# Performance work log

Measured on AMD Instinct MI355X. Metric: run time of the kernel, lower is better.

The kernel has to match this reference:

```python
import jax, jax.numpy as jnp
import numpy as np

N, B, I = 64, 32, 1
EMBED, ACT, DETER, STOCH, HIDDEN = 1536, 16, 2048, 512, 1024
EPS = 1e-5


def _ln(x, g, b):
    m = jnp.mean(x, -1, keepdims=True)
    v = jnp.mean((x - m) ** 2, -1, keepdims=True)
    return (x - m) / jnp.sqrt(v + EPS) * g + b


def setup_inputs() -> dict:
    key = jax.random.key(0)
    ks = jax.random.split(key, 24)
    s = 0.02
    d = {
        "embed": jax.random.normal(ks[0], (N, B, EMBED), jnp.float32),
        "action": jax.random.normal(ks[1], (N, B, ACT), jnp.float32),
        "reset": jnp.zeros((N, B), jnp.bool_),
        "h0": jnp.zeros((B * I, DETER), jnp.float32),
        "z0": jnp.zeros((B * I, STOCH), jnp.float32),
        "noises": jax.random.normal(ks[2], (N, B, I, STOCH), jnp.float32),
        # params
        "W_z": jax.random.normal(ks[3], (HIDDEN, STOCH)) * s,
        "b_z": jnp.zeros((HIDDEN,)),
        "W_a": jax.random.normal(ks[4], (HIDDEN, ACT)) * s,
        "ln_in_g": jnp.ones((HIDDEN,)), "ln_in_b": jnp.zeros((HIDDEN,)),
        "gru_Wih": jax.random.normal(ks[5], (3 * DETER, HIDDEN)) * s,
        "gru_Whh": jax.random.normal(ks[6], (3 * DETER, DETER)) * s,
        "gru_bih": jnp.zeros((3 * DETER,)), "gru_bhh": jnp.zeros((3 * DETER,)),
        "W_ph": jax.random.normal(ks[7], (HIDDEN, DETER)) * s,
        "b_ph": jnp.zeros((HIDDEN,)),
        "W_pe": jax.random.normal(ks[8], (HIDDEN, EMBED)) * s,
        "ln_post_g": jnp.ones((HIDDEN,)), "ln_post_b": jnp.zeros((HIDDEN,)),
        "W_post": jax.random.normal(ks[9], (2 * STOCH, HIDDEN)) * s,
        "b_post": jnp.zeros((2 * STOCH,)),
        "W_prh": jax.random.normal(ks[10], (HIDDEN, DETER)) * s,
        "b_prh": jnp.zeros((HIDDEN,)),
        "ln_pr_g": jnp.ones((HIDDEN,)), "ln_pr_b": jnp.zeros((HIDDEN,)),
        "W_pr": jax.random.normal(ks[11], (2 * STOCH, HIDDEN)) * s,
        "b_pr": jnp.zeros((2 * STOCH,)),
    }
    return d


def _core(embed, action, reset, h0, z0, noises,
          W_z, b_z, W_a, ln_in_g, ln_in_b,
          gru_Wih, gru_Whh, gru_bih, gru_bhh,
          W_ph, b_ph, W_pe, ln_post_g, ln_post_b, W_post, b_post,
          W_prh, b_prh, ln_pr_g, ln_pr_b, W_pr, b_pr):
    n, b = embed.shape[:2]
    # expand to (n, b*I, .) ; I == 1
    embeds = embed.reshape(n, b * I, -1)
    actions = action.reshape(n, b * I, -1)
    masks = (~reset).astype(jnp.float32).reshape(n, b * I, 1)
    noise = noises.reshape(n, b * I, -1)

    def step(carry, xs):
        h, z = carry
        e_t, a_t, m_t, n_t = xs
        h = h * m_t
        z = z * m_t
        x = z @ W_z.T + b_z + a_t @ W_a.T
        za = jax.nn.elu(_ln(x, ln_in_g, ln_in_b))
        # torch GRUCell
        gi = za @ gru_Wih.T + gru_bih
        gh = h @ gru_Whh.T + gru_bhh
        gi_r, gi_u, gi_n = jnp.split(gi, 3, -1)
        gh_r, gh_u, gh_n = jnp.split(gh, 3, -1)
        r = jax.nn.sigmoid(gi_r + gh_r)
        u = jax.nn.sigmoid(gi_u + gh_u)
        cand = jnp.tanh(gi_n + r * gh_n)
        h_new = (1.0 - u) * cand + u * h
        x = h_new @ W_ph.T + b_ph + e_t @ W_pe.T
        post_in = jax.nn.elu(_ln(x, ln_post_g, ln_post_b))
        post = post_in @ W_post.T + b_post
        mean, std_raw = jnp.split(post, 2, -1)
        std = jax.nn.softplus(std_raw) + 0.1
        sample = mean + std * n_t
        return (h_new, sample), (post, h_new, sample)

    (h_last, z_last), (posts, states_h, samples) = jax.lax.scan(
        step, (h0, z0), (embeds, actions, masks, noise))

    # batch prior over all h
    x = states_h @ W_prh.T + b_prh
    x = jax.nn.elu(_ln(x, ln_pr_g, ln_pr_b))
    priors = x @ W_pr.T + b_pr
    features = jnp.concatenate([states_h, samples], -1)

    rs = lambda t: t.reshape(n, b, I, -1)
    return rs(priors), rs(posts), rs(samples), rs(features), h_last, z_last


def reference(embed, action, reset, h0, z0, noises,
              W_z, b_z, W_a, ln_in_g, ln_in_b,
              gru_Wih, gru_Whh, gru_bih, gru_bhh,
              W_ph, b_ph, W_pe, ln_post_g, ln_post_b, W_post, b_post,
              W_prh, b_prh, ln_pr_g, ln_pr_b, W_pr, b_pr):
    return _core(embed, action, reset, h0, z0, noises,
                 W_z, b_z, W_a, ln_in_g, ln_in_b,
                 gru_Wih, gru_Whh, gru_bih, gru_bhh,
                 W_ph, b_ph, W_pe, ln_post_g, ln_post_b, W_post, b_post,
                 W_prh, b_prh, ln_pr_g, ln_pr_b, W_pr, b_pr)
```

## Files before the change

kernel.cpp:

```cpp
#include <hip/hip_runtime.h>
#include <hip/hip_bf16.h>
#include <stdint.h>

#define NSTEP 64
#define BATCH 32
#define EMBED_D 1536
#define ACT_D 16
#define DETER 2048
#define STOCH 512
#define HIDDEN 1024
#define FEAT 2560
#define NBLK 256

typedef __attribute__((ext_vector_type(8))) short bf16x8;
typedef __attribute__((ext_vector_type(4))) float f32x4;

#define MFMA16 __builtin_amdgcn_mfma_f32_16x16x32_bf16
#define AGENT __HIP_MEMORY_SCOPE_AGENT

__device__ __forceinline__ float eluf(float x) { return x > 0.f ? x : expf(x) - 1.f; }
__device__ __forceinline__ float sigf(float x) { return 1.f / (1.f + expf(-x)); }
__device__ __forceinline__ unsigned short f2bf(float f) {
    __hip_bfloat16 h = __float2bfloat16(f);
    return __builtin_bit_cast(unsigned short, h);
}
__device__ __forceinline__ float bf2f(unsigned short u) {
    unsigned v = ((unsigned)u) << 16;
    return __builtin_bit_cast(float, v);
}

__device__ __forceinline__ void stc_u32(unsigned* p, unsigned v) {
    __hip_atomic_store(p, v, __ATOMIC_RELAXED, AGENT);
}
__device__ __forceinline__ void stc_u64(unsigned long long* p, unsigned long long v) {
    __hip_atomic_store(p, v, __ATOMIC_RELAXED, AGENT);
}
__device__ __forceinline__ unsigned long long ldc_u64(const unsigned long long* p) {
    return __hip_atomic_load(p, __ATOMIC_RELAXED, AGENT);
}
__device__ __forceinline__ float ldc_f32(const float* p) {
    return __hip_atomic_load(p, __ATOMIC_RELAXED, AGENT);
}
__device__ __forceinline__ int ldc_i32(const int* p) {
    return __hip_atomic_load(p, __ATOMIC_RELAXED, AGENT);
}
__device__ __forceinline__ void stc_i32(int* p, int v) {
    __hip_atomic_store(p, v, __ATOMIC_RELAXED, AGENT);
}
__device__ __forceinline__ bf16x8 ldc_bf8(const unsigned short* p) {
    union { unsigned long long q[2]; bf16x8 v; } u;
    u.q[0] = ldc_u64((const unsigned long long*)p);
    u.q[1] = ldc_u64((const unsigned long long*)(p + 4));
    return u.v;
}
__device__ __forceinline__ ushort4 ldc_us4(const unsigned short* p) {
    unsigned long long q = ldc_u64((const unsigned long long*)p);
    return __builtin_bit_cast(ushort4, q);
}

__device__ __forceinline__ void gbar3(int* flags, int* release, int epoch) {
    asm volatile("s_waitcnt vmcnt(0)" ::: "memory");
    __syncthreads();
    if (blockIdx.x == 0) {
        int tid = threadIdx.x;
        if (tid >= 1 && tid < NBLK) {
            while (ldc_i32(&flags[tid * 32]) < epoch) __builtin_amdgcn_s_sleep(4);
        }
        asm volatile("" ::: "memory");
        __syncthreads();
        if (tid < 32) stc_i32(&release[tid * 32], epoch);
    } else {
        if (threadIdx.x == 0) {
            stc_i32(&flags[blockIdx.x * 32], epoch);
            int* rel = &release[(blockIdx.x & 31) * 32];
            while (ldc_i32(rel) < epoch) __builtin_amdgcn_s_sleep(4);
        }
        asm volatile("" ::: "memory");
        __syncthreads();
    }
}

__global__ __launch_bounds__(256) void k_cvt_all(
    const float* __restrict__ s0, unsigned short* __restrict__ d0,
    const float* __restrict__ s1, unsigned short* __restrict__ d1,
    const float* __restrict__ s2, unsigned short* __restrict__ d2,
    const float* __restrict__ s3, unsigned short* __restrict__ d3,
    const float* __restrict__ s4, unsigned short* __restrict__ d4)
{
    long long e = ((long long)blockIdx.x * 256 + threadIdx.x) * 4;
    const float* src; unsigned short* dst; long long off;
    if (e < 524288)        { src = s0; dst = d0; off = e; }
    else if (e < 6815744)  { src = s1; dst = d1; off = e - 524288; }
    else if (e < 19398656) { src = s2; dst = d2; off = e - 6815744; }
    else if (e < 21495808) { src = s3; dst = d3; off = e - 19398656; }
    else if (e < 22544384) { src = s4; dst = d4; off = e - 21495808; }
    else return;
    float4 v = *reinterpret_cast<const float4*>(src + off);
    ushort4 o;
    o.x = f2bf(v.x); o.y = f2bf(v.y); o.z = f2bf(v.z); o.w = f2bf(v.w);
    *reinterpret_cast<ushort4*>(dst + off) = o;
}

__global__ __launch_bounds__(256) void k_setup(
    const float* __restrict__ h0, const float* __restrict__ z0,
    const uint8_t* __restrict__ reset0,
    float* __restrict__ h0m, unsigned short* __restrict__ h16m0,
    unsigned short* __restrict__ z16m, int* __restrict__ flags)
{
    int gid = blockIdx.x * 256 + threadIdx.x;
    int idx = gid * 4;
    if (idx < BATCH * DETER) {
        int b = idx >> 11;
        float m = reset0[b] ? 0.f : 1.f;
        float4 v = *reinterpret_cast<const float4*>(h0 + idx);
        v.x *= m; v.y *= m; v.z *= m; v.w *= m;
        *reinterpret_cast<float4*>(h0m + idx) = v;
        ushort4 o;
        o.x = f2bf(v.x); o.y = f2bf(v.y); o.z = f2bf(v.z); o.w = f2bf(v.w);
        *reinterpret_cast<ushort4*>(h16m0 + idx) = o;
    } else if (idx < BATCH * DETER + BATCH * STOCH) {
        int zi = idx - BATCH * DETER;
        int b = zi >> 9;
        float m = reset0[b] ? 0.f : 1.f;
        float4 v = *reinterpret_cast<const float4*>(z0 + zi);
        ushort4 o;
        o.x = f2bf(v.x * m); o.y = f2bf(v.y * m); o.z = f2bf(v.z * m); o.w = f2bf(v.w * m);
        *reinterpret_cast<ushort4*>(z16m + zi) = o;
    }
    if (gid < 9216) flags[gid] = 0;
}

__global__ __launch_bounds__(256) void k_preA(
    const float* __restrict__ action, const float* __restrict__ Wa,
    const float* __restrict__ bz, float* __restrict__ preA)
{
    __shared__ float al[16];
    int r = blockIdx.x, t = threadIdx.x;
    if (t < 16) al[t] = action[r * 16 + t];
    __syncthreads();
#pragma unroll
    for (int c = 0; c < 4; ++c) {
        int j = t + c * 256;
        const float* wr = Wa + j * 16;
        float s = bz[j];
#pragma unroll
        for (int k = 0; k < 16; ++k) s += al[k] * wr[k];
        preA[(size_t)r * 1024 + j] = s;
    }
}

__global__ __launch_bounds__(256) void gemm_mfma(
    const float* __restrict__ A, int lda,
    const float* __restrict__ B, int ldb,
    const float* __restrict__ bias,
    float* __restrict__ C, int ldc, int K)
{
    __shared__ unsigned short Alds[64 * 72];
    __shared__ unsigned short Blds[64 * 72];
    int t = threadIdx.x;
    int nb = blockIdx.x, mb = blockIdx.y;
    int w = t >> 6, l = t & 63, l15 = l & 15, kg = l >> 4;
    f32x4 acc[4] = {{0,0,0,0},{0,0,0,0},{0,0,0,0},{0,0,0,0}};
    int srow = t >> 2, skq = (t & 3) * 16;
    const float* Asrc = A + (size_t)(mb * 64 + srow) * lda + skq;
    const float* Bsrc = B + (size_t)(nb * 64 + srow) * ldb + skq;
    unsigned short* Adst = &Alds[srow * 72 + skq];
    unsigned short* Bdst = &Blds[srow * 72 + skq];
    for (int kt = 0; kt < K; kt += 64) {
        __syncthreads();
#pragma unroll
        for (int c = 0; c < 16; c += 4) {
            float4 va = *reinterpret_cast<const float4*>(Asrc + kt + c);
            float4 vb = *reinterpret_cast<const float4*>(Bsrc + kt + c);
            ushort4 oa, ob;
            oa.x = f2bf(va.x); oa.y = f2bf(va.y); oa.z = f2bf(va.z); oa.w = f2bf(va.w);
            ob.x = f2bf(vb.x); ob.y = f2bf(vb.y); ob.z = f2bf(vb.z); ob.w = f2bf(vb.w);
            *reinterpret_cast<ushort4*>(Adst + c) = oa;
            *reinterpret_cast<ushort4*>(Bdst + c) = ob;
        }
        __syncthreads();
#pragma unroll
        for (int ks = 0; ks < 2; ks++) {
            bf16x8 a = *reinterpret_cast<const bf16x8*>(&Alds[(w * 16 + l15) * 72 + ks * 32 + kg * 8]);
#pragma unroll
            for (int nt = 0; nt < 4; nt++) {
                bf16x8 b = *reinterpret_cast<const bf16x8*>(&Blds[(nt * 16 + l15) * 72 + ks * 32 + kg * 8]);
                acc[nt] = MFMA16(a, b, acc[nt], 0, 0, 0);
            }
        }
    }
#pragma unroll
    for (int nt = 0; nt < 4; nt++) {
        int n = nb * 64 + nt * 16 + l15;
        float bv = bias[n];
#pragma unroll
        for (int i = 0; i < 4; i++) {
            C[(size_t)(mb * 64 + w * 16 + kg * 4 + i) * ldc + n] = acc[nt][i] + bv;
        }
    }
}

__global__ __launch_bounds__(256) void ln_elu_rows(
    float* __restrict__ X, const float* __restrict__ g, const float* __restrict__ bb)
{
    __shared__ float sbuf[256], qbuf[256];
    int r = blockIdx.x, t = threadIdx.x;
    float* row = X + (size_t)r * HIDDEN;
    float4 v = reinterpret_cast<const float4*>(row)[t];
    sbuf[t] = (v.x + v.y) + (v.z + v.w);
    qbuf[t] = (v.x * v.x + v.y * v.y) + (v.z * v.z + v.w * v.w);
    __syncthreads();
    for (int off = 128; off > 0; off >>= 1) {
        if (t < off) { sbuf[t] += sbuf[t + off]; qbuf[t] += qbuf[t + off]; }
        __syncthreads();
    }
    float mean = sbuf[0] / HIDDEN;
    float var = qbuf[0] / HIDDEN - mean * mean;
    float rstd = rsqrtf(var + 1e-5f);
    float4 gg = reinterpret_cast<const float4*>(g)[t];
    float4 bv = reinterpret_cast<const float4*>(bb)[t];
    float4 o;
    o.x = eluf((v.x - mean) * rstd * gg.x + bv.x);
    o.y = eluf((v.y - mean) * rstd * gg.y + bv.y);
    o.z = eluf((v.z - mean) * rstd * gg.z + bv.z);
    o.w = eluf((v.w - mean) * rstd * gg.w + bv.w);
    reinterpret_cast<float4*>(row)[t] = o;
}

__global__ __launch_bounds__(256) void k_copy_last(
    const float* __restrict__ feat63, const float* __restrict__ samp63,
    float* __restrict__ hlast, float* __restrict__ zlast)
{
    int i = blockIdx.x * 256 + threadIdx.x;
    if (i < BATCH * DETER) {
        int b = i / DETER, k = i % DETER;
        hlast[i] = feat63[(size_t)b * FEAT + k];
    }
    if (i < BATCH * STOCH) zlast[i] = samp63[i];
}

struct ScanArgs {
    const unsigned short *Wz16, *Wih16, *Whh16, *Wph16, *Wpo16;
    const float *bih, *bhh, *b_post;
    const float *ln_in_g, *ln_in_b, *ln_post_g, *ln_post_b;
    const float *h0m;
    const uint8_t *reset;
    const float *noises;
    float *postsPreA, *priorsPreE, *samples, *feats;
    unsigned short *z16m, *x1b, *x2b, *h16u, *h16m0, *h16m1;
    float *x1parts, *x2parts;
    int *flags, *release;
};

__device__ __forceinline__ void ln_stats(const float* __restrict__ parts, float* stat, int tid) {
    if (tid < 32) {
        float s = 0.f, q = 0.f;
        for (int i = 0; i < 64; ++i) {
            union { unsigned long long u; float f[2]; } c;
            c.u = ldc_u64((const unsigned long long*)(parts + (size_t)(i * 32 + tid) * 2));
            s += c.f[0]; q += c.f[1];
        }
        float mean = s * (1.f / 1024.f);
        float var = q * (1.f / 1024.f) - mean * mean;
        stat[tid] = mean;
        stat[32 + tid] = rsqrtf(var + 1e-5f);
    }
}

__device__ __forceinline__ void ln_fill(unsigned short* Asm, const unsigned short* __restrict__ src,
                                        const float* __restrict__ g, const float* __restrict__ bb,
                                        const float* stat, int tid) {
    int row = tid & 31, kb = (tid >> 5) * 128;
    float mean = stat[row], rstd = stat[32 + row];
#pragma unroll 4
    for (int c = 0; c < 16; ++c) {
        int k = kb + c * 8;
        ushort4 u0 = ldc_us4(src + (size_t)row * 1024 + k);
        ushort4 u1 = ldc_us4(src + (size_t)row * 1024 + k + 4);
        float4 g0 = *reinterpret_cast<const float4*>(g + k);
        float4 g1 = *reinterpret_cast<const float4*>(g + k + 4);
        float4 b0 = *reinterpret_cast<const float4*>(bb + k);
        float4 b1 = *reinterpret_cast<const float4*>(bb + k + 4);
        ushort4 o0, o1;
        o0.x = f2bf(eluf((bf2f(u0.x) - mean) * rstd * g0.x + b0.x));
        o0.y = f2bf(eluf((bf2f(u0.y) - mean) * rstd * g0.y + b0.y));
        o0.z = f2bf(eluf((bf2f(u0.z) - mean) * rstd * g0.z + b0.z));
        o0.w = f2bf(eluf((bf2f(u0.w) - mean) * rstd * g0.w + b0.w));
        o1.x = f2bf(eluf((bf2f(u1.x) - mean) * rstd * g1.x + b1.x));
        o1.y = f2bf(eluf((bf2f(u1.y) - mean) * rstd * g1.y + b1.y));
        o1.z = f2bf(eluf((bf2f(u1.z) - mean) * rstd * g1.z + b1.z));
        o1.w = f2bf(eluf((bf2f(u1.w) - mean) * rstd * g1.w + b1.w));
        *reinterpret_cast<ushort4*>(Asm + row * 1032 + k) = o0;
        *reinterpret_cast<ushort4*>(Asm + row * 1032 + k + 4) = o1;
    }
}

__global__ __launch_bounds__(512, 1) void k_scan(ScanArgs a) {
    __shared__ char smem[93184];
    unsigned short* Asm = (unsigned short*)smem;
    float* cbuf  = (float*)(smem + 66048);
    float* stat  = (float*)(smem + 66048 + 8192);
    float* stat2 = (float*)(smem + 90624);
    float* hbuf  = (float*)(smem + 91136);

    const int bid = blockIdx.x;
    const int tid = threadIdx.x;
    const int w = tid >> 6, l = tid & 63, l15 = l & 15, kg = l >> 4;
    int epoch = 0;

    for (int t = 0; t < NSTEP; ++t) {
        const float* preA_t = a.postsPreA + (size_t)t * 32768;
        const float* preE_t = a.priorsPreE + (size_t)t * 32768;
        float* posts_t = a.postsPreA + (size_t)t * 32768;
        float* samples_t = a.samples + (size_t)t * 16384;
        float* feats_t = a.feats + (size_t)t * 81920;
        const float* featsPrev = a.feats + (size_t)(t - 1) * 81920;
        const unsigned short* h16cur = (t & 1) ? a.h16m1 : a.h16m0;
        unsigned short* h16nxt = (t & 1) ? a.h16m0 : a.h16m1;

        if (bid < 64) {
            int j0 = bid * 16;
            if (tid < 256) {
                const unsigned short* A0 = a.z16m + l15 * 512 + w * 128 + kg * 8;
                const unsigned short* A1 = A0 + 16 * 512;
                const unsigned short* Bp = a.Wz16 + (size_t)(j0 + l15) * 512 + w * 128 + kg * 8;
                f32x4 c0 = {0,0,0,0}, c1 = {0,0,0,0};
#pragma unroll
                for (int ks = 0; ks < 4; ++ks) {
                    bf16x8 b = *reinterpret_cast<const bf16x8*>(Bp + ks * 32);
                    c0 = MFMA16(ldc_bf8(A0 + ks * 32), b, c0, 0, 0, 0);
                    c1 = MFMA16(ldc_bf8(A1 + ks * 32), b, c1, 0, 0, 0);
                }
#pragma unroll
                for (int i = 0; i < 4; ++i) {
                    cbuf[w * 512 + (kg * 4 + i) * 16 + l15] = c0[i];
                    cbuf[w * 512 + (16 + kg * 4 + i) * 16 + l15] = c1[i];
                }
            }
            __syncthreads();
            if (tid < 256) {
                int r = tid >> 3, c2 = (tid & 7) * 2;
                int base = r * 16 + c2;
                float v0 = cbuf[base] + cbuf[512 + base] + cbuf[1024 + base] + cbuf[1536 + base]
                         + preA_t[r * 1024 + j0 + c2];
                float v1 = cbuf[base + 1] + cbuf[512 + base + 1] + cbuf[1024 + base + 1] + cbuf[1536 + base + 1]
                         + preA_t[r * 1024 + j0 + c2 + 1];
                unsigned short u0 = f2bf(v0), u1 = f2bf(v1);
                stc_u32((unsigned*)(a.x1b + (size_t)r * 1024 + j0 + c2),
                        (unsigned)u0 | ((unsigned)u1 << 16));
                float w0 = bf2f(u0), w1 = bf2f(u1);
                float s = w0 + w1, q = w0 * w0 + w1 * w1;
                s += __shfl_xor(s, 1); q += __shfl_xor(q, 1);
                s += __shfl_xor(s, 2); q += __shfl_xor(q, 2);
                s += __shfl_xor(s, 4); q += __shfl_xor(q, 4);
                if ((tid & 7) == 0) {
                    union { float f[2]; unsigned long long u; } pu;
                    pu.f[0] = s; pu.f[1] = q;
                    stc_u64((unsigned long long*)(a.x1parts + ((size_t)bid * 32 + r) * 2), pu.u);
                }
            }
        }
        epoch++; gbar3(a.flags, a.release, epoch);

        if (bid < 128) {
            int j0 = bid * 16;
            ln_stats(a.x1parts, stat2, tid);
            __syncthreads();
            if (tid < 256) ln_fill(Asm, a.x1b, a.ln_in_g, a.ln_in_b, stat2, tid);
            __syncthreads();
            f32x4 cr = {0,0,0,0}, cu = {0,0,0,0}, cn = {0,0,0,0};
            if (w < 4) {
                int rowgrp = w & 1, kh = w >> 1;
                const unsigned short* ap = Asm + (rowgrp * 16 + l15) * 1032 + kh * 512 + kg * 8;
                const unsigned short* br = a.Wih16 + (size_t)(j0 + l15) * 1024 + kh * 512 + kg * 8;
                const unsigned short* bu = br + (size_t)2048 * 1024;
                const unsigned short* bn = bu + (size_t)2048 * 1024;
#pragma unroll 4
                for (int ks = 0; ks < 16; ++ks) {
                    bf16x8 av = *reinterpret_cast<const bf16x8*>(ap + ks * 32);
                    cr = MFMA16(av, *reinterpret_cast<const bf16x8*>(br + ks * 32), cr, 0, 0, 0);
                    cu = MFMA16(av, *reinterpret_cast<const bf16x8*>(bu + ks * 32), cu, 0, 0, 0);
                    cn = MFMA16(av, *reinterpret_cast<const bf16x8*>(bn + ks * 32), cn, 0, 0, 0);
                }
            } else {
                int idx = w - 4, rowgrp = idx & 1, kh = idx >> 1;
                const unsigned short* hp = h16cur + (size_t)(rowgrp * 16 + l15) * 2048 + kh * 1024 + kg * 8;
                const unsigned short* br = a.Whh16 + (size_t)(j0 + l15) * 2048 + kh * 1024 + kg * 8;
                const unsigned short* bu = br + (size_t)2048 * 2048;
                const unsigned short* bn = bu + (size_t)2048 * 2048;
#pragma unroll 4
                for (int ks = 0; ks < 32; ++ks) {
                    bf16x8 av = ldc_bf8(hp + ks * 32);
                    cr = MFMA16(av, *reinterpret_cast<const bf16x8*>(br + ks * 32), cr, 0, 0, 0);
                    cu = MFMA16(av, *reinterpret_cast<const bf16x8*>(bu + ks * 32), cu, 0, 0, 0);
                    cn = MFMA16(av, *reinterpret_cast<const bf16x8*>(bn + ks * 32), cn, 0, 0, 0);
                }
            }
#pragma unroll
            for (int i = 0; i < 4; ++i) {
                int o = (kg * 4 + i) * 16 + l15;
                cbuf[w * 768 + 0 * 256 + o] = cr[i];
                cbuf[w * 768 + 1 * 256 + o] = cu[i];
                cbuf[w * 768 + 2 * 256 + o] = cn[i];
            }
            __syncthreads();
            {
                int row = tid >> 4, col = tid & 15;
                int rowgrp = row >> 4, rr = row & 15;
                int o = rr * 16 + col;
                int j = j0 + col;
                float gr = cbuf[rowgrp * 768 + 0 * 256 + o] + cbuf[(2 + rowgrp) * 768 + 0 * 256 + o] + a.bih[j];
                float gu = cbuf[rowgrp * 768 + 1 * 256 + o] + cbuf[(2 + rowgrp) * 768 + 1 * 256 + o] + a.bih[j + 2048];
                float gn = cbuf[rowgrp * 768 + 2 * 256 + o] + cbuf[(2 + rowgrp) * 768 + 2 * 256 + o] + a.bih[j + 4096];
                float hr = cbuf[(4 + rowgrp) * 768 + 0 * 256 + o] + cbuf[(6 + rowgrp) * 768 + 0 * 256 + o] + a.bhh[j];
                float hu = cbuf[(4 + rowgrp) * 768 + 1 * 256 + o] + cbuf[(6 + rowgrp) * 768 + 1 * 256 + o] + a.bhh[j + 2048];
                float hn = cbuf[(4 + rowgrp) * 768 + 2 * 256 + o] + cbuf[(6 + rowgrp) * 768 + 2 * 256 + o] + a.bhh[j + 4096];
                float r_ = sigf(gr + hr), u_ = sigf(gu + hu);
                float cand = tanhf(gn + r_ * hn);
                float m = a.reset[t * 32 + row] ? 0.f : 1.f;
                float hpv = (t == 0) ? a.h0m[(size_t)row * 2048 + j]
                                     : ldc_f32(featsPrev + (size_t)row * 2560 + j);
                hbuf[row * 16 + col] = (1.f - u_) * cand + u_ * (m * hpv);
            }
            __syncthreads();
            if (tid < 256) {
                int b = tid >> 3, c2 = (tid & 7) * 2;
                float h0v = hbuf[b * 16 + c2], h1v = hbuf[b * 16 + c2 + 1];
                int j = j0 + c2;
                union { float f[2]; unsigned long long u; } fu;
                fu.f[0] = h0v; fu.f[1] = h1v;
                stc_u64((unsigned long long*)(feats_t + (size_t)b * 2560 + j), fu.u);
                unsigned short g0 = f2bf(h0v), g1 = f2bf(h1v);
                stc_u32((unsigned*)(a.h16u + (size_t)b * 2048 + j),
                        (unsigned)g0 | ((unsigned)g1 << 16));
                float mn = (t < 63) ? (a.reset[(t + 1) * 32 + b] ? 0.f : 1.f) : 1.f;
                unsigned short n0 = f2bf(h0v * mn), n1 = f2bf(h1v * mn);
                stc_u32((unsigned*)(h16nxt + (size_t)b * 2048 + j),
                        (unsigned)n0 | ((unsigned)n1 << 16));
            }
        }
        epoch++; gbar3(a.flags, a.release, epoch);

        if (bid < 64) {
            int j0 = bid * 16;
            if (tid < 256) {
                const unsigned short* A0 = a.h16u + l15 * 2048 + w * 512 + kg * 8;
                const unsigned short* A1 = A0 + 16 * 2048;
                const unsigned short* Bp = a.Wph16 + (size_t)(j0 + l15) * 2048 + w * 512 + kg * 8;
                f32x4 c0 = {0,0,0,0}, c1 = {0,0,0,0};
#pragma unroll 8
                for (int ks = 0; ks < 16; ++ks) {
                    bf16x8 b = *reinterpret_cast<const bf16x8*>(Bp + ks * 32);
                    c0 = MFMA16(ldc_bf8(A0 + ks * 32), b, c0, 0, 0, 0);
                    c1 = MFMA16(ldc_bf8(A1 + ks * 32), b, c1, 0, 0, 0);
                }
#pragma unroll
                for (int i = 0; i < 4; ++i) {
                    cbuf[w * 512 + (kg * 4 + i) * 16 + l15] = c0[i];
                    cbuf[w * 512 + (16 + kg * 4 + i) * 16 + l15] = c1[i];
                }
            }
            __syncthreads();
            if (tid < 256) {
                int r = tid >> 3, c2 = (tid & 7) * 2;
                int base = r * 16 + c2;
                float v0 = cbuf[base] + cbuf[512 + base] + cbuf[1024 + base] + cbuf[1536 + base]
                         + preE_t[r * 1024 + j0 + c2];
                float v1 = cbuf[base + 1] + cbuf[512 + base + 1] + cbuf[1024 + base + 1] + cbuf[1536 + base + 1]
                         + preE_t[r * 1024 + j0 + c2 + 1];
                unsigned short u0 = f2bf(v0), u1 = f2bf(v1);
                stc_u32((unsigned*)(a.x2b + (size_t)r * 1024 + j0 + c2),
                        (unsigned)u0 | ((unsigned)u1 << 16));
                float w0 = bf2f(u0), w1 = bf2f(u1);
                float s = w0 + w1, q = w0 * w0 + w1 * w1;
                s += __shfl_xor(s, 1); q += __shfl_xor(q, 1);
                s += __shfl_xor(s, 2); q += __shfl_xor(q, 2);
                s += __shfl_xor(s, 4); q += __shfl_xor(q, 4);
                if ((tid & 7) == 0) {
                    union { float f[2]; unsigned long long u; } pu;
                    pu.f[0] = s; pu.f[1] = q;
                    stc_u64((unsigned long long*)(a.x2parts + ((size_t)bid * 32 + r) * 2), pu.u);
                }
            }
        }
        epoch++; gbar3(a.flags, a.release, epoch);

        if (bid < 32) {
            int j0 = bid * 16;
            ln_stats(a.x2parts, stat, tid);
            __syncthreads();
            if (tid < 256) ln_fill(Asm, a.x2b, a.ln_post_g, a.ln_post_b, stat, tid);
            __syncthreads();
            if (tid < 256) {
                int tile = w >> 1, mt = w & 1;
                const unsigned short* ap = Asm + (mt * 16 + l15) * 1032 + kg * 8;
                int n = (tile == 0) ? (j0 + l15) : (512 + j0 + l15);
                const unsigned short* Bp = a.Wpo16 + (size_t)n * 1024 + kg * 8;
                f32x4 c = {0,0,0,0};
#pragma unroll 8
                for (int ks = 0; ks < 32; ++ks) {
                    c = MFMA16(*reinterpret_cast<const bf16x8*>(ap + ks * 32),
                               *reinterpret_cast<const bf16x8*>(Bp + ks * 32), c, 0, 0, 0);
                }
#pragma unroll
                for (int i = 0; i < 4; ++i)
                    cbuf[(tile * 2 + mt) * 256 + (kg * 4 + i) * 16 + l15] = c[i];
            }
            __syncthreads();
            if (tid < 256) {
                int b = tid >> 3, c2 = (tid & 7) * 2;
                int j = j0 + c2;
                int ib = (b >> 4) * 256 + (b & 15) * 16;
                float pm0 = cbuf[ib + c2] + a.b_post[j];
                float pm1 = cbuf[ib + c2 + 1] + a.b_post[j + 1];
                float ps0 = cbuf[512 + ib + c2] + a.b_post[512 + j];
                float ps1 = cbuf[512 + ib + c2 + 1] + a.b_post[512 + j + 1];
                posts_t[(size_t)b * 1024 + j] = pm0;
                posts_t[(size_t)b * 1024 + j + 1] = pm1;
                posts_t[(size_t)b * 1024 + 512 + j] = ps0;
                posts_t[(size_t)b * 1024 + 512 + j + 1] = ps1;
                float sp0 = fmaxf(ps0, 0.f) + log1pf(expf(-fabsf(ps0)));
                float sp1 = fmaxf(ps1, 0.f) + log1pf(expf(-fabsf(ps1)));
                float n0v = a.noises[(size_t)t * 16384 + b * 512 + j];
                float n1v = a.noises[(size_t)t * 16384 + b * 512 + j + 1];
                float smp0 = pm0 + (sp0 + 0.1f) * n0v;
                float smp1 = pm1 + (sp1 + 0.1f) * n1v;
                samples_t[(size_t)b * 512 + j] = smp0;
                samples_t[(size_t)b * 512 + j + 1] = smp1;
                feats_t[(size_t)b * 2560 + 2048 + j] = smp0;
                feats_t[(size_t)b * 2560 + 2048 + j + 1] = smp1;
                float mn = (t < 63) ? (a.reset[(t + 1) * 32 + b] ? 0.f : 1.f) : 1.f;
                unsigned short z0_ = f2bf(smp0 * mn), z1_ = f2bf(smp1 * mn);
                stc_u32((unsigned*)(a.z16m + (size_t)b * 512 + j),
                        (unsigned)z0_ | ((unsigned)z1_ << 16));
            }
        }
        epoch++; gbar3(a.flags, a.release, epoch);
    }
}

#define WS_WZ16   ((size_t)0)
#define WS_WIH16  ((size_t)1048576)
#define WS_WHH16  ((size_t)13631488)
#define WS_WPH16  ((size_t)38797312)
#define WS_WPO16  ((size_t)42991616)
#define WS_Z16M   ((size_t)45088768)
#define WS_H16M0  ((size_t)45121536)
#define WS_H16M1  ((size_t)45252608)
#define WS_H16U   ((size_t)45383680)
#define WS_H0M    ((size_t)45514752)
#define WS_X1B    ((size_t)45776896)
#define WS_X2B    ((size_t)45842432)
#define WS_X1P    ((size_t)45907968)
#define WS_X2P    ((size_t)45924352)
#define WS_FLAGS  ((size_t)45940736)
#define WS_REL    ((size_t)45973504)
#define WS_PRX    WS_WIH16

extern "C" void kernel_launch(void* const* d_in, const int* in_sizes, int n_in,
                              void* d_out, int out_size, void* d_ws, size_t ws_size,
                              hipStream_t stream)
{
    (void)in_sizes; (void)n_in; (void)out_size; (void)ws_size;
    const float*   embed  = (const float*)d_in[0];
    const float*   action = (const float*)d_in[1];
    const uint8_t* reset  = (const uint8_t*)d_in[2];
    const float*   h0     = (const float*)d_in[3];
    const float*   z0     = (const float*)d_in[4];
    const float*   noises = (const float*)d_in[5];
    const float*   W_z    = (const float*)d_in[6];
    const float*   b_z    = (const float*)d_in[7];
    const float*   W_a    = (const float*)d_in[8];
    const float*   ln_in_g = (const float*)d_in[9];
    const float*   ln_in_b = (const float*)d_in[10];
    const float*   Wih    = (const float*)d_in[11];
    const float*   Whh    = (const float*)d_in[12];
    const float*   bih    = (const float*)d_in[13];
    const float*   bhh    = (const float*)d_in[14];
    const float*   W_ph   = (const float*)d_in[15];
    const float*   b_ph   = (const float*)d_in[16];
    const float*   W_pe   = (const float*)d_in[17];
    const float*   ln_post_g = (const float*)d_in[18];
    const float*   ln_post_b = (const float*)d_in[19];
    const float*   W_post = (const float*)d_in[20];
    const float*   b_post = (const float*)d_in[21];
    const float*   W_prh  = (const float*)d_in[22];
    const float*   b_prh  = (const float*)d_in[23];
    const float*   ln_pr_g = (const float*)d_in[24];
    const float*   ln_pr_b = (const float*)d_in[25];
    const float*   W_pr   = (const float*)d_in[26];
    const float*   b_pr   = (const float*)d_in[27];

    float* out     = (float*)d_out;
    float* priors  = out;
    float* posts   = out + 2097152;
    float* samples = out + 4194304;
    float* feats   = out + 5242880;
    float* hlast   = out + 10485760;
    float* zlast   = out + 10551296;

    char* ws = (char*)d_ws;
    unsigned short* Wz16  = (unsigned short*)(ws + WS_WZ16);
    unsigned short* Wih16 = (unsigned short*)(ws + WS_WIH16);
    unsigned short* Whh16 = (unsigned short*)(ws + WS_WHH16);
    unsigned short* Wph16 = (unsigned short*)(ws + WS_WPH16);
    unsigned short* Wpo16 = (unsigned short*)(ws + WS_WPO16);
    unsigned short* z16m  = (unsigned short*)(ws + WS_Z16M);
    unsigned short* h16m0 = (unsigned short*)(ws + WS_H16M0);
    unsigned short* h16m1 = (unsigned short*)(ws + WS_H16M1);
    unsigned short* h16u  = (unsigned short*)(ws + WS_H16U);
    float*          h0m   = (float*)(ws + WS_H0M);
    unsigned short* x1b   = (unsigned short*)(ws + WS_X1B);
    unsigned short* x2b   = (unsigned short*)(ws + WS_X2B);
    float*          x1p   = (float*)(ws + WS_X1P);
    float*          x2p   = (float*)(ws + WS_X2P);
    int*            flags = (int*)(ws + WS_FLAGS);
    int*            release = (int*)(ws + WS_REL);
    float*          prx   = (float*)(ws + WS_PRX);

    dim3 blk(256);

    k_cvt_all<<<dim3(22016), blk, 0, stream>>>(W_z, Wz16, Wih, Wih16, Whh, Whh16,
                                               W_ph, Wph16, W_post, Wpo16);
    k_setup<<<dim3(80), blk, 0, stream>>>(h0, z0, reset, h0m, h16m0, z16m, flags);

    k_preA<<<dim3(2048), blk, 0, stream>>>(action, W_a, b_z, posts);
    gemm_mfma<<<dim3(16, 32), blk, 0, stream>>>(embed, EMBED_D, W_pe, EMBED_D, b_ph,
                                                priors, HIDDEN, EMBED_D);

    ScanArgs sa;
    sa.Wz16 = Wz16; sa.Wih16 = Wih16; sa.Whh16 = Whh16; sa.Wph16 = Wph16; sa.Wpo16 = Wpo16;
    sa.bih = bih; sa.bhh = bhh; sa.b_post = b_post;
    sa.ln_in_g = ln_in_g; sa.ln_in_b = ln_in_b; sa.ln_post_g = ln_post_g; sa.ln_post_b = ln_post_b;
    sa.h0m = h0m; sa.reset = reset; sa.noises = noises;
    sa.postsPreA = posts; sa.priorsPreE = priors; sa.samples = samples; sa.feats = feats;
    sa.z16m = z16m; sa.x1b = x1b; sa.x2b = x2b; sa.h16u = h16u;
    sa.h16m0 = h16m0; sa.h16m1 = h16m1;
    sa.x1parts = x1p; sa.x2parts = x2p;
    sa.flags = flags; sa.release = release;

    k_scan<<<dim3(NBLK), dim3(512), 0, stream>>>(sa);

    gemm_mfma<<<dim3(16, 32), blk, 0, stream>>>(feats, FEAT, W_prh, DETER, b_prh,
                                                prx, HIDDEN, DETER);
    ln_elu_rows<<<dim3(2048), blk, 0, stream>>>(prx, ln_pr_g, ln_pr_b);
    gemm_mfma<<<dim3(16, 32), blk, 0, stream>>>(prx, HIDDEN, W_pr, HIDDEN, b_pr,
                                                priors, HIDDEN, HIDDEN);

    k_copy_last<<<dim3(256), blk, 0, stream>>>(
        feats + (size_t)(NSTEP - 1) * BATCH * FEAT,
        samples + (size_t)(NSTEP - 1) * BATCH * STOCH,
        hlast, zlast);
}
```

Before: 4.510 ms.

## Spread LN stats, LN fill and small GEMMs across all 512 threads

LayerNorm statistics reduction is now split across all threads with a shared-memory second-stage sum, replacing the 32-thread serial loop over 64 partials. The LN fill and the posterior-head and W_ph GEMMs now use all 8 waves by splitting the K dimension, with partial sums combined in shared memory. This targets the serial latency inside each step of the scan's critical path, at the cost of extra LDS traffic and reduction work.

```diff
diff --git a/kernel.cpp b/kernel.cpp
--- a/kernel.cpp
+++ b/kernel.cpp
@@ -252,28 +252,40 @@
     int *flags, *release;
 };
 
-__device__ __forceinline__ void ln_stats(const float* __restrict__ parts, float* stat, int tid) {
+__device__ __forceinline__ void ln_stats2(const float* __restrict__ parts, float* stat,
+                                          float* scratch, int tid) {
+    int row = tid & 31, grp = tid >> 5;
+    float s = 0.f, q = 0.f;
+#pragma unroll
+    for (int i = 0; i < 4; ++i) {
+        union { unsigned long long u; float f[2]; } c;
+        c.u = ldc_u64((const unsigned long long*)parts + (size_t)(grp * 4 + i) * 32 + row);
+        s += c.f[0]; q += c.f[1];
+    }
+    scratch[row * 16 + grp] = s;
+    scratch[512 + row * 16 + grp] = q;
+    __syncthreads();
     if (tid < 32) {
-        float s = 0.f, q = 0.f;
-        for (int i = 0; i < 64; ++i) {
-            union { unsigned long long u; float f[2]; } c;
-            c.u = ldc_u64((const unsigned long long*)(parts + (size_t)(i * 32 + tid) * 2));
-            s += c.f[0]; q += c.f[1];
-        }
-        float mean = s * (1.f / 1024.f);
-        float var = q * (1.f / 1024.f) - mean * mean;
+        float ss = 0.f, qq = 0.f;
+#pragma unroll
+        for (int g = 0; g < 16; ++g) {
+            ss += scratch[tid * 16 + g];
+            qq += scratch[512 + tid * 16 + g];
+        }
+        float mean = ss * (1.f / 1024.f);
+        float var = qq * (1.f / 1024.f) - mean * mean;
         stat[tid] = mean;
         stat[32 + tid] = rsqrtf(var + 1e-5f);
     }
 }
 
-__device__ __forceinline__ void ln_fill(unsigned short* Asm, const unsigned short* __restrict__ src,
-                                        const float* __restrict__ g, const float* __restrict__ bb,
-                                        const float* stat, int tid) {
-    int row = tid & 31, kb = (tid >> 5) * 128;
+__device__ __forceinline__ void ln_fill512(unsigned short* Asm, const unsigned short* __restrict__ src,
+                                           const float* __restrict__ g, const float* __restrict__ bb,
+                                           const float* stat, int tid) {
+    int row = tid & 31, kb = (tid >> 5) * 64;
     float mean = stat[row], rstd = stat[32 + row];
-#pragma unroll 4
-    for (int c = 0; c < 16; ++c) {
+#pragma unroll 2
+    for (int c = 0; c < 8; ++c) {
         int k = kb + c * 8;
         ushort4 u0 = ldc_us4(src + (size_t)row * 1024 + k);
         ushort4 u1 = ldc_us4(src + (size_t)row * 1024 + k + 4);
@@ -364,9 +376,9 @@
 
         if (bid < 128) {
             int j0 = bid * 16;
-            ln_stats(a.x1parts, stat2, tid);
-            __syncthreads();
-            if (tid < 256) ln_fill(Asm, a.x1b, a.ln_in_g, a.ln_in_b, stat2, tid);
+            ln_stats2(a.x1parts, stat2, cbuf, tid);
+            __syncthreads();
+            ln_fill512(Asm, a.x1b, a.ln_in_g, a.ln_in_b, stat2, tid);
             __syncthreads();
             f32x4 cr = {0,0,0,0}, cu = {0,0,0,0}, cn = {0,0,0,0};
             if (w < 4) {
@@ -443,31 +455,32 @@
 
         if (bid < 64) {
             int j0 = bid * 16;
-            if (tid < 256) {
-                const unsigned short* A0 = a.h16u + l15 * 2048 + w * 512 + kg * 8;
-                const unsigned short* A1 = A0 + 16 * 2048;
-                const unsigned short* Bp = a.Wph16 + (size_t)(j0 + l15) * 2048 + w * 512 + kg * 8;
-                f32x4 c0 = {0,0,0,0}, c1 = {0,0,0,0};
-#pragma unroll 8
+            {
+                int rowgrp = w & 1, kq = w >> 1;
+                const unsigned short* Ap = a.h16u + (size_t)(rowgrp * 16 + l15) * 2048 + kq * 512 + kg * 8;
+                const unsigned short* Bp = a.Wph16 + (size_t)(j0 + l15) * 2048 + kq * 512 + kg * 8;
+                f32x4 c0 = {0,0,0,0};
+#pragma unroll 4
                 for (int ks = 0; ks < 16; ++ks) {
-                    bf16x8 b = *reinterpret_cast<const bf16x8*>(Bp + ks * 32);
-                    c0 = MFMA16(ldc_bf8(A0 + ks * 32), b, c0, 0, 0, 0);
-                    c1 = MFMA16(ldc_bf8(A1 + ks * 32), b, c1, 0, 0, 0);
-                }
-#pragma unroll
-                for (int i = 0; i < 4; ++i) {
-                    cbuf[w * 512 + (kg * 4 + i) * 16 + l15] = c0[i];
-                    cbuf[w * 512 + (16 + kg * 4 + i) * 16 + l15] = c1[i];
-                }
+                    c0 = MFMA16(ldc_bf8(Ap + ks * 32),
+                                *reinterpret_cast<const bf16x8*>(Bp + ks * 32), c0, 0, 0, 0);
+                }
+#pragma unroll
+                for (int i = 0; i < 4; ++i)
+                    cbuf[w * 256 + (kg * 4 + i) * 16 + l15] = c0[i];
             }
             __syncthreads();
             if (tid < 256) {
                 int r = tid >> 3, c2 = (tid & 7) * 2;
-                int base = r * 16 + c2;
-                float v0 = cbuf[base] + cbuf[512 + base] + cbuf[1024 + base] + cbuf[1536 + base]
-                         + preE_t[r * 1024 + j0 + c2];
-                float v1 = cbuf[base + 1] + cbuf[512 + base + 1] + cbuf[1024 + base + 1] + cbuf[1536 + base + 1]
-                         + preE_t[r * 1024 + j0 + c2 + 1];
+                int rowgrp2 = r >> 4, rr = r & 15;
+                float v0 = 0.f, v1 = 0.f;
+#pragma unroll
+                for (int kq2 = 0; kq2 < 4; ++kq2) {
+                    v0 += cbuf[(kq2 * 2 + rowgrp2) * 256 + rr * 16 + c2];
+                    v1 += cbuf[(kq2 * 2 + rowgrp2) * 256 + rr * 16 + c2 + 1];
+                }
+                v0 += preE_t[(size_t)r * 1024 + j0 + c2];
+                v1 += preE_t[(size_t)r * 1024 + j0 + c2 + 1];
                 unsigned short u0 = f2bf(v0), u1 = f2bf(v1);
                 stc_u32((unsigned*)(a.x2b + (size_t)r * 1024 + j0 + c2),
                         (unsigned)u0 | ((unsigned)u1 << 16));
@@ -487,34 +500,34 @@
 
         if (bid < 32) {
             int j0 = bid * 16;
-            ln_stats(a.x2parts, stat, tid);
-            __syncthreads();
-            if (tid < 256) ln_fill(Asm, a.x2b, a.ln_post_g, a.ln_post_b, stat, tid);
-            __syncthreads();
-            if (tid < 256) {
-                int tile = w >> 1, mt = w & 1;
-                const unsigned short* ap = Asm + (mt * 16 + l15) * 1032 + kg * 8;
-                int n = (tile == 0) ? (j0 + l15) : (512 + j0 + l15);
-                const unsigned short* Bp = a.Wpo16 + (size_t)n * 1024 + kg * 8;
+            ln_stats2(a.x2parts, stat, cbuf, tid);
+            __syncthreads();
+            ln_fill512(Asm, a.x2b, a.ln_post_g, a.ln_post_b, stat, tid);
+            __syncthreads();
+            {
+                int tile = w >> 2, mt = (w >> 1) & 1, kh = w & 1;
+                const unsigned short* ap = Asm + (mt * 16 + l15) * 1032 + kh * 512 + kg * 8;
+                int n = tile ? (512 + j0 + l15) : (j0 + l15);
+                const unsigned short* Bp = a.Wpo16 + (size_t)n * 1024 + kh * 512 + kg * 8;
                 f32x4 c = {0,0,0,0};
-#pragma unroll 8
-                for (int ks = 0; ks < 32; ++ks) {
+#pragma unroll 4
+                for (int ks = 0; ks < 16; ++ks) {
                     c = MFMA16(*reinterpret_cast<const bf16x8*>(ap + ks * 32),
                                *reinterpret_cast<const bf16x8*>(Bp + ks * 32), c, 0, 0, 0);
                 }
 #pragma unroll
                 for (int i = 0; i < 4; ++i)
-                    cbuf[(tile * 2 + mt) * 256 + (kg * 4 + i) * 16 + l15] = c[i];
+                    cbuf[w * 256 + (kg * 4 + i) * 16 + l15] = c[i];
             }
             __syncthreads();
             if (tid < 256) {
                 int b = tid >> 3, c2 = (tid & 7) * 2;
                 int j = j0 + c2;
-                int ib = (b >> 4) * 256 + (b & 15) * 16;
-                float pm0 = cbuf[ib + c2] + a.b_post[j];
-                float pm1 = cbuf[ib + c2 + 1] + a.b_post[j + 1];
-                float ps0 = cbuf[512 + ib + c2] + a.b_post[512 + j];
-                float ps1 = cbuf[512 + ib + c2 + 1] + a.b_post[512 + j + 1];
+                int mt2 = b >> 4, rr = b & 15, o = rr * 16;
+                float pm0 = cbuf[(mt2 * 2 + 0) * 256 + o + c2] + cbuf[(mt2 * 2 + 1) * 256 + o + c2] + a.b_post[j];
+                float pm1 = cbuf[(mt2 * 2 + 0) * 256 + o + c2 + 1] + cbuf[(mt2 * 2 + 1) * 256 + o + c2 + 1] + a.b_post[j + 1];
+                float ps0 = cbuf[(4 + mt2 * 2 + 0) * 256 + o + c2] + cbuf[(4 + mt2 * 2 + 1) * 256 + o + c2] + a.b_post[512 + j];
+                float ps1 = cbuf[(4 + mt2 * 2 + 0) * 256 + o + c2 + 1] + cbuf[(4 + mt2 * 2 + 1) * 256 + o + c2 + 1] + a.b_post[512 + j + 1];
                 posts_t[(size_t)b * 1024 + j] = pm0;
                 posts_t[(size_t)b * 1024 + j + 1] = pm1;
                 posts_t[(size_t)b * 1024 + 512 + j] = ps0;
```

After: 4.353 ms. 3.5% less time.
